# Kernel tuning notes

Hardware: AMD Instinct MI355X
Metric: run time of the kernel (lower is better)

The kernel has to match this reference:

```python
import jax, jax.numpy as jnp
import numpy as np

N = 50000
E = 600000
D = 128
EPS = 1e-5  # nn.LayerNorm default eps


def gcn_conv(x, W, b, src, dst):
    # PyG GCNConv with add_self_loops=True, edge_weight=None (all ones),
    # symmetric normalization D^-1/2 (A+I) D^-1/2.
    h = x @ W                                        # [N, D]
    deg = jnp.zeros((N,), h.dtype).at[dst].add(1.0) + 1.0  # +1 for self loop
    dinv = jax.lax.rsqrt(deg)                        # deg >= 1, safe
    norm = dinv[src] * dinv[dst]                     # [E]
    msg = h[src] * norm[:, None]                     # [E, D] gather
    agg = jax.ops.segment_sum(msg, dst, num_segments=N)
    agg = agg + h * (dinv * dinv)[:, None]           # self-loop term
    return agg + b


def layer_norm(x, g, b):
    mu = jnp.mean(x, axis=-1, keepdims=True)
    var = jnp.mean(jnp.square(x - mu), axis=-1, keepdims=True)
    return (x - mu) * jax.lax.rsqrt(var + EPS) * g + b


def setup_inputs() -> dict:
    key = jax.random.key(0)
    ks = jax.random.split(key, 6)
    x = jax.random.normal(ks[0], (N, D), dtype=jnp.float32)
    edge_index = jax.random.randint(ks[1], (2, E), 0, N, dtype=jnp.int64)
    s = 1.0 / np.sqrt(D)
    W1 = jax.random.uniform(ks[2], (D, D), jnp.float32, -s, s)
    W2 = jax.random.uniform(ks[3], (D, D), jnp.float32, -s, s)
    b1 = jnp.zeros((D,), jnp.float32)
    b2 = jnp.zeros((D,), jnp.float32)
    ln1_g = jnp.ones((D,), jnp.float32)
    ln1_b = jnp.zeros((D,), jnp.float32)
    ln2_g = jnp.ones((D,), jnp.float32)
    ln2_b = jnp.zeros((D,), jnp.float32)
    return {"x": x, "edge_index": edge_index, "W1": W1, "b1": b1,
            "ln1_g": ln1_g, "ln1_b": ln1_b, "W2": W2, "b2": b2,
            "ln2_g": ln2_g, "ln2_b": ln2_b}


def reference(x, edge_index, W1, b1, ln1_g, ln1_b, W2, b2, ln2_g, ln2_b):
    src, dst = edge_index[0], edge_index[1]
    out = gcn_conv(x, W1, b1, src, dst)
    out = jax.nn.relu(layer_norm(out, ln1_g, ln1_b))  # dropout = identity (eval)
    out = gcn_conv(out, W2, b2, src, dst)
    out = jax.nn.relu(layer_norm(out, ln2_g, ln2_b))
    return out + x
```

## Files before the change

kernel.cpp:

```cpp
#include <hip/hip_runtime.h>
#include <hip/hip_fp16.h>

#define D 128
#define EPS 1e-5f
#define KB 256
#define KBSH 8
#define NBSH 7
#define BUCKW 128

typedef unsigned int u32;
typedef unsigned short u16;
typedef unsigned char u8;
typedef __attribute__((ext_vector_type(8))) _Float16 half8;
typedef __attribute__((ext_vector_type(4))) float f32x4;
typedef __attribute__((ext_vector_type(2))) float f32x2;

__device__ inline u16 f2h(float x) {
  _Float16 t = (_Float16)x;
  return __builtin_bit_cast(u16, t);
}
__device__ inline u8 f2fp8(float x) {
  return (u8)(__builtin_amdgcn_cvt_pk_fp8_f32(x, x, 0, false) & 0xff);
}

__global__ __launch_bounds__(256) void k_prep(const float* __restrict__ W1,
                                              const float* __restrict__ W2,
                                              u16* __restrict__ Wt1,
                                              u16* __restrict__ Wt2) {
  int i = blockIdx.x * 256 + threadIdx.x;
  if (i < 2 * D * D) {
    const float* W = (i < D * D) ? W1 : W2;
    u16* Wt = (i < D * D) ? Wt1 : Wt2;
    int ii = i & (D * D - 1);
    int k = ii >> 7, c = ii & 127;
    Wt[c * D + k] = f2h(W[ii]);
  }
}

template <bool F32IN>
__device__ __forceinline__ void gemm_body(const void* __restrict__ in_,
                                          const u16* __restrict__ Wt,
                                          u8* __restrict__ out, int nrows,
                                          int blk, u16 (*sA)[136]) {
  const int tid = threadIdx.x;

  if (F32IN) {
    const float* in = (const float*)in_;
#pragma unroll
    for (int r = 0; r < 2; r++) {
      int c = tid + r * 256;
      int row = c >> 4, col8 = c & 15;
      int rg = min(blk * 32 + row, nrows - 1);
      float4 v0 = *(const float4*)(in + (size_t)rg * D + col8 * 8);
      float4 v1 = *(const float4*)(in + (size_t)rg * D + col8 * 8 + 4);
      half8 h;
      h[0] = (_Float16)v0.x; h[1] = (_Float16)v0.y;
      h[2] = (_Float16)v0.z; h[3] = (_Float16)v0.w;
      h[4] = (_Float16)v1.x; h[5] = (_Float16)v1.y;
      h[6] = (_Float16)v1.z; h[7] = (_Float16)v1.w;
      *(half8*)(&sA[row][col8 * 8]) = h;
    }
  } else {
    const u16* in = (const u16*)in_;
#pragma unroll
    for (int r = 0; r < 2; r++) {
      int c = tid + r * 256;
      int row = c >> 4, col8 = c & 15;
      int rg = min(blk * 32 + row, nrows - 1);
      *(half8*)(&sA[row][col8 * 8]) =
          *(const half8*)(in + (size_t)rg * D + col8 * 8);
    }
  }
  __syncthreads();

  const int lane = tid & 63, wv = tid >> 6;
  const int m = lane & 15, q = lane >> 4;
  const int rl0 = (wv & 1) * 16;
  const int ch = wv >> 1;

  f32x4 acc[4];
#pragma unroll
  for (int c = 0; c < 4; c++) acc[c] = (f32x4)(0.0f);

#pragma unroll
  for (int kk = 0; kk < 4; kk++) {
    const int kbase = kk * 32 + q * 8;
    half8 a = *(const half8*)(&sA[rl0 + m][kbase]);
#pragma unroll
    for (int c = 0; c < 4; c++) {
      int ct = ch * 4 + c;
      half8 b = *(const half8*)(Wt + (ct * 16 + m) * D + kbase);
      acc[c] = __builtin_amdgcn_mfma_f32_16x16x32_f16(a, b, acc[c], 0, 0, 0);
    }
  }
  __syncthreads();

  u8* so = (u8*)sA;
#pragma unroll
  for (int c = 0; c < 4; c++) {
    int ct = ch * 4 + c;
#pragma unroll
    for (int rg = 0; rg < 4; rg++) {
      so[(rl0 + q * 4 + rg) * 144 + ct * 16 + m] = f2fp8(acc[c][rg]);
    }
  }
  __syncthreads();

  {
    int row = tid >> 3, col16 = tid & 7;
    int rr = blk * 32 + row;
    if (rr < nrows) {
      uint4 v = *(const uint4*)(so + row * 144 + col16 * 16);
      *(uint4*)(out + (size_t)rr * D + col16 * 16) = v;
    }
  }
}

__global__ __launch_bounds__(256) void k_count_gemm1(
    const int* __restrict__ dst, int* __restrict__ cnt, int E, int NB, int EPB,
    const float* __restrict__ x, const u16* __restrict__ Wt1,
    u8* __restrict__ A, int nrows) {
  __shared__ int hist[512];
  __shared__ alignas(16) u16 sA[32][136];
  if (blockIdx.x < (u32)KB) {
    const int k = blockIdx.x, tid = threadIdx.x;
    for (int i = tid; i < NB; i += 256) hist[i] = 0;
    __syncthreads();
    const int e0 = k * EPB, e1 = min(E, e0 + EPB);
    for (int base = e0 + tid; base < e1; base += 2048) {
      int dd[8];
#pragma unroll
      for (int i = 0; i < 8; i++) {
        int e = base + i * 256;
        dd[i] = (e < e1) ? dst[e] : -1;
      }
#pragma unroll
      for (int i = 0; i < 8; i++)
        if (dd[i] >= 0) atomicAdd(&hist[dd[i] >> NBSH], 1);
    }
    __syncthreads();
    for (int b = tid; b < NB; b += 256) cnt[b * KB + k] = hist[b];
  } else {
    gemm_body<true>(x, Wt1, A, nrows, blockIdx.x - KB, sA);
  }
}

__global__ __launch_bounds__(256) void k_scan_reduce(
    const int* __restrict__ cnt, int M, int* __restrict__ bsum) {
  const int b = blockIdx.x, t = threadIdx.x;
  const int lane = t & 63, w = t >> 6;
  int idx = b * 1024 + t * 4;
  int4 v = make_int4(0, 0, 0, 0);
  if (idx + 3 < M) {
    v = *(const int4*)(cnt + idx);
  } else {
    if (idx + 0 < M) v.x = cnt[idx + 0];
    if (idx + 1 < M) v.y = cnt[idx + 1];
    if (idx + 2 < M) v.z = cnt[idx + 2];
  }
  int s = v.x + v.y + v.z + v.w;
#pragma unroll
  for (int o = 1; o < 64; o <<= 1) s += __shfl_xor(s, o, 64);
  __shared__ int ws[4];
  if (lane == 0) ws[w] = s;
  __syncthreads();
  if (t == 0) bsum[b] = ws[0] + ws[1] + ws[2] + ws[3];
}

__global__ __launch_bounds__(256) void k_scan_apply(
    int* __restrict__ cnt, int M, const int* __restrict__ bsum,
    int* __restrict__ bsv, int NB, int E) {
  const int b = blockIdx.x, t = threadIdx.x;
  const int lane = t & 63, w = t >> 6;
  if (b == 0 && t == 0) bsv[NB] = E;
  int idx = b * 1024 + t * 4;
  int4 v = make_int4(0, 0, 0, 0);
  if (idx + 3 < M) {
    v = *(const int4*)(cnt + idx);
  } else {
    if (idx + 0 < M) v.x = cnt[idx + 0];
    if (idx + 1 < M) v.y = cnt[idx + 1];
    if (idx + 2 < M) v.z = cnt[idx + 2];
  }
  int s = v.x + v.y + v.z + v.w;
  int incl = s;
#pragma unroll
  for (int o = 1; o < 64; o <<= 1) {
    int u = __shfl_up(incl, o, 64);
    if (lane >= o) incl += u;
  }
  __shared__ int ws[4];
  __shared__ int sboff;
  if (lane == 63) ws[w] = incl;
  if (t < 64) {
    int partial = 0;
    for (int j = t; j < b; j += 64) partial += bsum[j];
#pragma unroll
    for (int o = 32; o >= 1; o >>= 1) partial += __shfl_xor(partial, o, 64);
    if (t == 0) sboff = partial;
  }
  __syncthreads();
  int wbase = 0;
#pragma unroll
  for (int j = 0; j < 4; j++)
    if (j < w) wbase += ws[j];
  int base = sboff + wbase + incl - s;
  int e0 = base, e1 = e0 + v.x, e2 = e1 + v.y, e3 = e2 + v.z;
  if (idx < M) {
    cnt[idx] = e0;
    if ((idx & (KB - 1)) == 0) bsv[idx >> KBSH] = e0;
  }
  if (idx + 1 < M) cnt[idx + 1] = e1;
  if (idx + 2 < M) cnt[idx + 2] = e2;
  if (idx + 3 < M) cnt[idx + 3] = e3;
}

__global__ __launch_bounds__(256) void k_scatter(
    const int* __restrict__ src, const int* __restrict__ dst,
    const int* __restrict__ cnt, u32* __restrict__ tmp, int E, int NB,
    int EPB) {
  __shared__ int off[512];
  const int k = blockIdx.x, tid = threadIdx.x;
  for (int b = tid; b < NB; b += 256) off[b] = cnt[b * KB + k];
  __syncthreads();
  const int e0 = k * EPB, e1 = min(E, e0 + EPB);
  for (int base = e0 + tid; base < e1; base += 2048) {
    int dd[8], ss[8];
#pragma unroll
    for (int i = 0; i < 8; i++) {
      int e = base + i * 256;
      dd[i] = (e < e1) ? dst[e] : -1;
      ss[i] = (e < e1) ? src[e] : 0;
    }
#pragma unroll
    for (int i = 0; i < 8; i++) {
      if (dd[i] >= 0) {
        int p = atomicAdd(&off[dd[i] >> NBSH], 1);
        tmp[p] = (u32)ss[i] | ((u32)(dd[i] & (BUCKW - 1)) << 16);
      }
    }
  }
}

__global__ __launch_bounds__(256) void k_bucket(
    const u32* __restrict__ tmp, const int* __restrict__ bsv,
    int4* __restrict__ meta, float* __restrict__ dinv,
    u32* __restrict__ csr, int N) {
  __shared__ int hist[BUCKW];
  __shared__ int sc[BUCKW];
  __shared__ int cur[BUCKW];
  const int b = blockIdx.x, tid = threadIdx.x;
  const int s0 = bsv[b], s1 = bsv[b + 1];
  if (tid < BUCKW) hist[tid] = 0;
  __syncthreads();
  for (int base = s0 + tid; base < s1; base += 1024) {
    int tt[4];
#pragma unroll
    for (int i = 0; i < 4; i++) {
      int idx = base + i * 256;
      tt[i] = (idx < s1) ? (int)tmp[idx] : -1;
    }
#pragma unroll
    for (int i = 0; i < 4; i++)
      if (tt[i] >= 0) atomicAdd(&hist[(tt[i] >> 16) & (BUCKW - 1)], 1);
  }
  __syncthreads();
  if (tid < BUCKW) sc[tid] = hist[tid];
  __syncthreads();
#pragma unroll
  for (int o = 1; o < BUCKW; o <<= 1) {
    int t = 0;
    if (tid < BUCKW && tid >= o) t = sc[tid - o];
    __syncthreads();
    if (tid < BUCKW) sc[tid] += t;
    __syncthreads();
  }
  if (tid < BUCKW) {
    int dg = hist[tid];
    int excl = sc[tid] - dg;
    cur[tid] = excl;
    int d = (b << NBSH) + tid;
    if (d < N) {
      float dv = rsqrtf((float)dg + 1.0f);
      meta[d] = make_int4(s0 + excl, dg, __builtin_bit_cast(int, dv), 0);
      dinv[d] = dv;
    }
  }
  __syncthreads();
  for (int base = s0 + tid; base < s1; base += 1024) {
    int tt[4];
#pragma unroll
    for (int i = 0; i < 4; i++) {
      int idx = base + i * 256;
      tt[i] = (idx < s1) ? (int)tmp[idx] : -1;
    }
#pragma unroll
    for (int i = 0; i < 4; i++) {
      if (tt[i] >= 0) {
        int r = atomicAdd(&cur[(tt[i] >> 16) & (BUCKW - 1)], 1);
        csr[s0 + r] = (u32)tt[i] & 0xffffu;
      }
    }
  }
}

#define ACC_EDGE(vv, ww)                                                     \
  {                                                                          \
    f32x2 p_;                                                                \
    p_ = __builtin_amdgcn_cvt_pk_f32_fp8(vv.x, false);                       \
    acc[0] = fmaf(p_[0], ww, acc[0]); acc[1] = fmaf(p_[1], ww, acc[1]);      \
    p_ = __builtin_amdgcn_cvt_pk_f32_fp8(vv.x, true);                        \
    acc[2] = fmaf(p_[0], ww, acc[2]); acc[3] = fmaf(p_[1], ww, acc[3]);      \
    p_ = __builtin_amdgcn_cvt_pk_f32_fp8(vv.y, false);                       \
    acc[4] = fmaf(p_[0], ww, acc[4]); acc[5] = fmaf(p_[1], ww, acc[5]);      \
    p_ = __builtin_amdgcn_cvt_pk_f32_fp8(vv.y, true);                        \
    acc[6] = fmaf(p_[0], ww, acc[6]); acc[7] = fmaf(p_[1], ww, acc[7]);      \
  }

__device__ __forceinline__ void gather_ln_core(
    const uint2* __restrict__ hb, const int4* __restrict__ meta,
    const u32* __restrict__ csr, const float* __restrict__ dinv,
    const float* __restrict__ b,
    const float* __restrict__ g, const float* __restrict__ bln,
    int row, int n, int sl, float out[8]) {
  const bool valid = row < n;
  const int rc = valid ? row : 0;
  int4 mt = meta[rc];
  int beg = mt.x;
  int cnt = valid ? mt.y : 0;
  float dv = __builtin_bit_cast(float, mt.z);
  float sn = dv * dv;

  float acc[8];
  {
    uint2 su = hb[(size_t)rc * 16 + sl];
    f32x2 p0 = __builtin_amdgcn_cvt_pk_f32_fp8(su.x, false);
    f32x2 p1 = __builtin_amdgcn_cvt_pk_f32_fp8(su.x, true);
    f32x2 p2 = __builtin_amdgcn_cvt_pk_f32_fp8(su.y, false);
    f32x2 p3 = __builtin_amdgcn_cvt_pk_f32_fp8(su.y, true);
    acc[0] = p0[0] * sn; acc[1] = p0[1] * sn;
    acc[2] = p1[0] * sn; acc[3] = p1[1] * sn;
    acc[4] = p2[0] * sn; acc[5] = p2[1] * sn;
    acc[6] = p3[0] * sn; acc[7] = p3[1] * sn;
  }

  for (int j0 = 0; j0 < cnt; j0 += 8) {
    u32 e[8];
#pragma unroll
    for (int jj = 0; jj < 8; jj++) {
      int j = j0 + jj;
      e[jj] = (j < cnt) ? csr[beg + j] : 0u;
    }
    uint2 v[8];
#pragma unroll
    for (int jj = 0; jj < 8; jj++)
      v[jj] = hb[(size_t)e[jj] * 16 + sl];
    float dw[8];
#pragma unroll
    for (int jj = 0; jj < 8; jj++) {
      int j = j0 + jj;
      dw[jj] = (j < cnt) ? dinv[e[jj]] : 0.0f;
    }
#pragma unroll
    for (int jj = 0; jj < 8; jj++) ACC_EDGE(v[jj], dw[jj] * dv);
  }

  int d0 = sl * 8;
  float4 bb0 = *(const float4*)(b + d0);
  float4 bb1 = *(const float4*)(b + d0 + 4);
  float a0 = acc[0] + bb0.x, a1 = acc[1] + bb0.y;
  float a2 = acc[2] + bb0.z, a3 = acc[3] + bb0.w;
  float a4 = acc[4] + bb1.x, a5 = acc[5] + bb1.y;
  float a6 = acc[6] + bb1.z, a7 = acc[7] + bb1.w;

  float sum = ((a0 + a1) + (a2 + a3)) + ((a4 + a5) + (a6 + a7));
#pragma unroll
  for (int o = 8; o >= 1; o >>= 1) sum += __shfl_xor(sum, o, 16);
  float mu = sum * (1.0f / 128.0f);
  float e0 = a0 - mu, e1 = a1 - mu, e2 = a2 - mu, e3 = a3 - mu;
  float e4 = a4 - mu, e5 = a5 - mu, e6 = a6 - mu, e7 = a7 - mu;
  float vs = ((e0 * e0 + e1 * e1) + (e2 * e2 + e3 * e3)) +
             ((e4 * e4 + e5 * e5) + (e6 * e6 + e7 * e7));
#pragma unroll
  for (int o = 8; o >= 1; o >>= 1) vs += __shfl_xor(vs, o, 16);
  float inv = rsqrtf(vs * (1.0f / 128.0f) + EPS);

  float4 gg0 = *(const float4*)(g + d0);
  float4 gg1 = *(const float4*)(g + d0 + 4);
  float4 bl0 = *(const float4*)(bln + d0);
  float4 bl1 = *(const float4*)(bln + d0 + 4);
  out[0] = fmaxf(e0 * inv * gg0.x + bl0.x, 0.0f);
  out[1] = fmaxf(e1 * inv * gg0.y + bl0.y, 0.0f);
  out[2] = fmaxf(e2 * inv * gg0.z + bl0.z, 0.0f);
  out[3] = fmaxf(e3 * inv * gg0.w + bl0.w, 0.0f);
  out[4] = fmaxf(e4 * inv * gg1.x + bl1.x, 0.0f);
  out[5] = fmaxf(e5 * inv * gg1.y + bl1.y, 0.0f);
  out[6] = fmaxf(e6 * inv * gg1.z + bl1.z, 0.0f);
  out[7] = fmaxf(e7 * inv * gg1.w + bl1.w, 0.0f);
}

__global__ __launch_bounds__(256, 8) void k_gather1(
    const uint2* __restrict__ hb, const int4* __restrict__ meta,
    const u32* __restrict__ csr, const float* __restrict__ dinv,
    const float* __restrict__ b, const float* __restrict__ g,
    const float* __restrict__ bln,
    u16* __restrict__ y1, int n) {
  const int tid = threadIdx.x;
  const int sl = tid & 15;
  const int row = blockIdx.x * 16 + (tid >> 4);
  float o[8];
  gather_ln_core(hb, meta, csr, dinv, b, g, bln, row, n, sl, o);
  if (row >= n) return;
  uint4 pk;
  pk.x = ((u32)f2h(o[1]) << 16) | (u32)f2h(o[0]);
  pk.y = ((u32)f2h(o[3]) << 16) | (u32)f2h(o[2]);
  pk.z = ((u32)f2h(o[5]) << 16) | (u32)f2h(o[4]);
  pk.w = ((u32)f2h(o[7]) << 16) | (u32)f2h(o[6]);
  *(uint4*)(y1 + (size_t)row * D + sl * 8) = pk;
}

__global__ __launch_bounds__(256) void k_gemm2(const u16* __restrict__ y1,
                                               const u16* __restrict__ Wt2,
                                               u8* __restrict__ outB, int n) {
  __shared__ alignas(16) u16 sA[32][136];
  gemm_body<false>(y1, Wt2, outB, n, blockIdx.x, sA);
}

__global__ __launch_bounds__(256, 8) void k_gather2(
    const uint2* __restrict__ hb, const int4* __restrict__ meta,
    const u32* __restrict__ csr, const float* __restrict__ dinv,
    const float* __restrict__ b, const float* __restrict__ g,
    const float* __restrict__ bln, const float* __restrict__ resid,
    float* __restrict__ outf, int n) {
  const int tid = threadIdx.x;
  const int sl = tid & 15;
  const int row = blockIdx.x * 16 + (tid >> 4);
  float o[8];
  gather_ln_core(hb, meta, csr, dinv, b, g, bln, row, n, sl, o);
  if (row >= n) return;
  size_t base = (size_t)row * D + sl * 8;
  f32x4 r0 = __builtin_nontemporal_load((const f32x4*)(resid + base));
  f32x4 r1 = __builtin_nontemporal_load((const f32x4*)(resid + base + 4));
  f32x4 w0, w1;
  w0[0] = o[0] + r0[0]; w0[1] = o[1] + r0[1];
  w0[2] = o[2] + r0[2]; w0[3] = o[3] + r0[3];
  w1[0] = o[4] + r1[0]; w1[1] = o[5] + r1[1];
  w1[2] = o[6] + r1[2]; w1[3] = o[7] + r1[3];
  __builtin_nontemporal_store(w0, (f32x4*)(outf + base));
  __builtin_nontemporal_store(w1, (f32x4*)(outf + base + 4));
}

extern "C" void kernel_launch(void* const* d_in, const int* in_sizes, int n_in,
                              void* d_out, int out_size, void* d_ws, size_t ws_size,
                              hipStream_t stream) {
  const float* x    = (const float*)d_in[0];
  const int*   ei   = (const int*)d_in[1];
  const float* W1   = (const float*)d_in[2];
  const float* b1   = (const float*)d_in[3];
  const float* g1   = (const float*)d_in[4];
  const float* bl1  = (const float*)d_in[5];
  const float* W2   = (const float*)d_in[6];
  const float* b2   = (const float*)d_in[7];
  const float* g2   = (const float*)d_in[8];
  const float* bl2  = (const float*)d_in[9];

  const int N = in_sizes[0] / D;
  const int E = in_sizes[1] / 2;
  const int* src = ei;
  const int* dst = ei + E;

  const int NB  = (N + BUCKW - 1) / BUCKW;
  const int M   = NB * KB;
  const int EPB = (E + KB - 1) / KB;
  const int GB  = (N + 31) / 32;
  const int RB  = (N + 15) / 16;
  const int SB  = (M + 1023) / 1024;

  size_t off = 0;
  auto walloc = [&](size_t bytes) {
    void* p = (char*)d_ws + off;
    off = (off + bytes + 255) & ~(size_t)255;
    return p;
  };
  int*   cnt   = (int*)walloc((size_t)M * 4);
  int*   bsum  = (int*)walloc((size_t)SB * 4);
  int*   bsv   = (int*)walloc((size_t)(NB + 1) * 4);
  u32*   tmp   = (u32*)walloc((size_t)E * 4);
  u32*   csr   = (u32*)walloc((size_t)E * 4);
  int4*  meta  = (int4*)walloc((size_t)N * 16);
  float* dinv  = (float*)walloc((size_t)N * 4);
  u8*    A     = (u8*)walloc((size_t)N * D);
  u8*    B     = (u8*)walloc((size_t)N * D);
  u16*   Wt1   = (u16*)walloc((size_t)D * D * 2);
  u16*   Wt2   = (u16*)walloc((size_t)D * D * 2);
  u16*   y1    = (u16*)walloc((size_t)N * D * 2);
  float* O     = (float*)d_out;

  k_prep<<<(2 * D * D + 255) / 256, 256, 0, stream>>>(W1, W2, Wt1, Wt2);
  k_count_gemm1<<<KB + GB, 256, 0, stream>>>(dst, cnt, E, NB, EPB, x, Wt1, A, N);
  k_scan_reduce<<<SB, 256, 0, stream>>>(cnt, M, bsum);
  k_scan_apply<<<SB, 256, 0, stream>>>(cnt, M, bsum, bsv, NB, E);
  k_scatter<<<KB, 256, 0, stream>>>(src, dst, cnt, tmp, E, NB, EPB);
  k_bucket<<<NB, 256, 0, stream>>>(tmp, bsv, meta, dinv, csr, N);
  k_gather1<<<RB, 256, 0, stream>>>((const uint2*)A, meta, csr, dinv,
                                    b1, g1, bl1, y1, N);
  k_gemm2<<<GB, 256, 0, stream>>>(y1, Wt2, B, N);
  k_gather2<<<RB, 256, 0, stream>>>((const uint2*)B, meta, csr, dinv,
                                    b2, g2, bl2, x, O, N);
}
```

Measured before the change: 182.7 us.

## Split neighbor gather into two source-range passes for cache locality

Each destination's CSR edge list is now partitioned by source index: low-half sources are packed from the front and high-half sources from the back, and the split count goes into meta.w. Each GCN aggregation becomes two kernels. The first gathers only low-half sources and writes fp32 partial sums to a new N×D buffer. The second gathers the high-half sources, adds the partials, and applies bias, LayerNorm and ReLU. The aim is to keep each pass's gathered feature working set smaller so it fits better in cache, at the cost of an extra fp32 partial write and read plus two more launches.

```diff
diff --git a/kernel.cpp b/kernel.cpp
--- a/kernel.cpp
+++ b/kernel.cpp
@@ -245,10 +245,11 @@
 __global__ __launch_bounds__(256) void k_bucket(
     const u32* __restrict__ tmp, const int* __restrict__ bsv,
     int4* __restrict__ meta, float* __restrict__ dinv,
-    u32* __restrict__ csr, int N) {
+    u32* __restrict__ csr, int N, int SLAB) {
   __shared__ int hist[BUCKW];
   __shared__ int sc[BUCKW];
-  __shared__ int cur[BUCKW];
+  __shared__ int curlo[BUCKW];
+  __shared__ int curhi[BUCKW];
   const int b = blockIdx.x, tid = threadIdx.x;
   const int s0 = bsv[b], s1 = bsv[b + 1];
   if (tid < BUCKW) hist[tid] = 0;
@@ -278,7 +279,8 @@
   if (tid < BUCKW) {
     int dg = hist[tid];
     int excl = sc[tid] - dg;
-    cur[tid] = excl;
+    curlo[tid] = excl;
+    curhi[tid] = excl + dg - 1;
     int d = (b << NBSH) + tid;
     if (d < N) {
       float dv = rsqrtf((float)dg + 1.0f);
@@ -297,9 +299,20 @@
 #pragma unroll
     for (int i = 0; i < 4; i++) {
       if (tt[i] >= 0) {
-        int r = atomicAdd(&cur[(tt[i] >> 16) & (BUCKW - 1)], 1);
-        csr[s0 + r] = (u32)tt[i] & 0xffffu;
+        int dl = (tt[i] >> 16) & (BUCKW - 1);
+        int sr = (int)((u32)tt[i] & 0xffffu);
+        int r = (sr < SLAB) ? atomicAdd(&curlo[dl], 1)
+                            : atomicSub(&curhi[dl], 1);
+        csr[s0 + r] = (u32)sr;
       }
+    }
+  }
+  __syncthreads();
+  if (tid < BUCKW) {
+    int d = (b << NBSH) + tid;
+    if (d < N) {
+      int excl = sc[tid] - hist[tid];
+      ((int*)meta)[d * 4 + 3] = curlo[tid] - excl;
     }
   }
 }
@@ -317,17 +330,37 @@
     acc[6] = fmaf(p_[0], ww, acc[6]); acc[7] = fmaf(p_[1], ww, acc[7]);      \
   }
 
-__device__ __forceinline__ void gather_ln_core(
+#define EDGE_LOOP(B0, CN)                                                    \
+  for (int j0 = 0; j0 < (CN); j0 += 8) {                                     \
+    u32 e[8];                                                                \
+    _Pragma("unroll") for (int jj = 0; jj < 8; jj++) {                       \
+      int j = j0 + jj;                                                       \
+      e[jj] = (j < (CN)) ? csr[(B0) + j] : 0u;                               \
+    }                                                                        \
+    uint2 v[8];                                                              \
+    _Pragma("unroll") for (int jj = 0; jj < 8; jj++)                         \
+        v[jj] = hb[(size_t)e[jj] * 16 + sl];                                 \
+    float dw[8];                                                             \
+    _Pragma("unroll") for (int jj = 0; jj < 8; jj++) {                       \
+      int j = j0 + jj;                                                       \
+      dw[jj] = (j < (CN)) ? dinv[e[jj]] : 0.0f;                              \
+    }                                                                        \
+    _Pragma("unroll") for (int jj = 0; jj < 8; jj++)                         \
+        ACC_EDGE(v[jj], dw[jj] * dv);                                        \
+  }
+
+__global__ __launch_bounds__(256, 8) void k_gather_a(
     const uint2* __restrict__ hb, const int4* __restrict__ meta,
     const u32* __restrict__ csr, const float* __restrict__ dinv,
-    const float* __restrict__ b,
-    const float* __restrict__ g, const float* __restrict__ bln,
-    int row, int n, int sl, float out[8]) {
+    float* __restrict__ P, int n) {
+  const int tid = threadIdx.x;
+  const int sl = tid & 15;
+  const int row = blockIdx.x * 16 + (tid >> 4);
   const bool valid = row < n;
   const int rc = valid ? row : 0;
   int4 mt = meta[rc];
   int beg = mt.x;
-  int cnt = valid ? mt.y : 0;
+  int c0 = valid ? mt.w : 0;
   float dv = __builtin_bit_cast(float, mt.z);
   float sn = dv * dv;
 
@@ -344,26 +377,43 @@
     acc[6] = p3[0] * sn; acc[7] = p3[1] * sn;
   }
 
-  for (int j0 = 0; j0 < cnt; j0 += 8) {
-    u32 e[8];
-#pragma unroll
-    for (int jj = 0; jj < 8; jj++) {
-      int j = j0 + jj;
-      e[jj] = (j < cnt) ? csr[beg + j] : 0u;
-    }
-    uint2 v[8];
-#pragma unroll
-    for (int jj = 0; jj < 8; jj++)
-      v[jj] = hb[(size_t)e[jj] * 16 + sl];
-    float dw[8];
-#pragma unroll
-    for (int jj = 0; jj < 8; jj++) {
-      int j = j0 + jj;
-      dw[jj] = (j < cnt) ? dinv[e[jj]] : 0.0f;
-    }
-#pragma unroll
-    for (int jj = 0; jj < 8; jj++) ACC_EDGE(v[jj], dw[jj] * dv);
-  }
+  EDGE_LOOP(beg, c0)
+
+  if (!valid) return;
+  f32x4 w0, w1;
+  w0[0] = acc[0]; w0[1] = acc[1]; w0[2] = acc[2]; w0[3] = acc[3];
+  w1[0] = acc[4]; w1[1] = acc[5]; w1[2] = acc[6]; w1[3] = acc[7];
+  size_t base = (size_t)row * D + sl * 8;
+  __builtin_nontemporal_store(w0, (f32x4*)(P + base));
+  __builtin_nontemporal_store(w1, (f32x4*)(P + base + 4));
+}
+
+__device__ __forceinline__ void gather_b_core(
+    const uint2* __restrict__ hb, const int4* __restrict__ meta,
+    const u32* __restrict__ csr, const float* __restrict__ dinv,
+    const float* __restrict__ P, const float* __restrict__ b,
+    const float* __restrict__ g, const float* __restrict__ bln,
+    int row, int n, int sl, float out[8]) {
+  const bool valid = row < n;
+  const int rc = valid ? row : 0;
+  int4 mt = meta[rc];
+  int beg = mt.x;
+  int cnt = valid ? mt.y : 0;
+  int c0 = valid ? mt.w : 0;
+  float dv = __builtin_bit_cast(float, mt.z);
+
+  float acc[8];
+  {
+    size_t base = (size_t)rc * D + sl * 8;
+    f32x4 r0 = __builtin_nontemporal_load((const f32x4*)(P + base));
+    f32x4 r1 = __builtin_nontemporal_load((const f32x4*)(P + base + 4));
+    acc[0] = r0[0]; acc[1] = r0[1]; acc[2] = r0[2]; acc[3] = r0[3];
+    acc[4] = r1[0]; acc[5] = r1[1]; acc[6] = r1[2]; acc[7] = r1[3];
+  }
+
+  const int b1 = beg + c0;
+  const int c1 = cnt - c0;
+  EDGE_LOOP(b1, c1)
 
   int d0 = sl * 8;
   float4 bb0 = *(const float4*)(b + d0);
@@ -399,9 +449,10 @@
   out[7] = fmaxf(e7 * inv * gg1.w + bl1.w, 0.0f);
 }
 
-__global__ __launch_bounds__(256, 8) void k_gather1(
+__global__ __launch_bounds__(256, 8) void k_g1b(
     const uint2* __restrict__ hb, const int4* __restrict__ meta,
     const u32* __restrict__ csr, const float* __restrict__ dinv,
+    const float* __restrict__ P,
     const float* __restrict__ b, const float* __restrict__ g,
     const float* __restrict__ bln,
     u16* __restrict__ y1, int n) {
@@ -409,7 +460,7 @@
   const int sl = tid & 15;
   const int row = blockIdx.x * 16 + (tid >> 4);
   float o[8];
-  gather_ln_core(hb, meta, csr, dinv, b, g, bln, row, n, sl, o);
+  gather_b_core(hb, meta, csr, dinv, P, b, g, bln, row, n, sl, o);
   if (row >= n) return;
   uint4 pk;
   pk.x = ((u32)f2h(o[1]) << 16) | (u32)f2h(o[0]);
@@ -426,9 +477,10 @@
   gemm_body<false>(y1, Wt2, outB, n, blockIdx.x, sA);
 }
 
-__global__ __launch_bounds__(256, 8) void k_gather2(
+__global__ __launch_bounds__(256, 8) void k_g2b(
     const uint2* __restrict__ hb, const int4* __restrict__ meta,
     const u32* __restrict__ csr, const float* __restrict__ dinv,
+    const float* __restrict__ P,
     const float* __restrict__ b, const float* __restrict__ g,
     const float* __restrict__ bln, const float* __restrict__ resid,
     float* __restrict__ outf, int n) {
@@ -436,7 +488,7 @@
   const int sl = tid & 15;
   const int row = blockIdx.x * 16 + (tid >> 4);
   float o[8];
-  gather_ln_core(hb, meta, csr, dinv, b, g, bln, row, n, sl, o);
+  gather_b_core(hb, meta, csr, dinv, P, b, g, bln, row, n, sl, o);
   if (row >= n) return;
   size_t base = (size_t)row * D + sl * 8;
   f32x4 r0 = __builtin_nontemporal_load((const f32x4*)(resid + base));
@@ -475,6 +527,7 @@
   const int GB  = (N + 31) / 32;
   const int RB  = (N + 15) / 16;
   const int SB  = (M + 1023) / 1024;
+  const int SLAB = (N + 1) / 2;
 
   size_t off = 0;
   auto walloc = [&](size_t bytes) {
@@ -494,6 +547,7 @@
   u16*   Wt1   = (u16*)walloc((size_t)D * D * 2);
   u16*   Wt2   = (u16*)walloc((size_t)D * D * 2);
   u16*   y1    = (u16*)walloc((size_t)N * D * 2);
+  float* P     = (float*)walloc((size_t)N * D * 4);
   float* O     = (float*)d_out;
 
   k_prep<<<(2 * D * D + 255) / 256, 256, 0, stream>>>(W1, W2, Wt1, Wt2);
@@ -501,10 +555,12 @@
   k_scan_reduce<<<SB, 256, 0, stream>>>(cnt, M, bsum);
   k_scan_apply<<<SB, 256, 0, stream>>>(cnt, M, bsum, bsv, NB, E);
   k_scatter<<<KB, 256, 0, stream>>>(src, dst, cnt, tmp, E, NB, EPB);
-  k_bucket<<<NB, 256, 0, stream>>>(tmp, bsv, meta, dinv, csr, N);
-  k_gather1<<<RB, 256, 0, stream>>>((const uint2*)A, meta, csr, dinv,
-                                    b1, g1, bl1, y1, N);
+  k_bucket<<<NB, 256, 0, stream>>>(tmp, bsv, meta, dinv, csr, N, SLAB);
+  k_gather_a<<<RB, 256, 0, stream>>>((const uint2*)A, meta, csr, dinv, P, N);
+  k_g1b<<<RB, 256, 0, stream>>>((const uint2*)A, meta, csr, dinv, P,
+                                b1, g1, bl1, y1, N);
   k_gemm2<<<GB, 256, 0, stream>>>(y1, Wt2, B, N);
-  k_gather2<<<RB, 256, 0, stream>>>((const uint2*)B, meta, csr, dinv,
-                                    b2, g2, bl2, x, O, N);
-}
+  k_gather_a<<<RB, 256, 0, stream>>>((const uint2*)B, meta, csr, dinv, P, N);
+  k_g2b<<<RB, 256, 0, stream>>>((const uint2*)B, meta, csr, dinv, P,
+                                b2, g2, bl2, x, O, N);
+}
```

Result: slower. 208.7 us (+14.2%).
